# Kernel tuning notes

Measured on AMD Instinct MI355X. Metric: run time of the kernel, lower is better.

The kernel has to match this reference:

```python
import jax, jax.numpy as jnp
import numpy as np

N, E, F, B = 4096, 8192, 256, 16


def setup_inputs() -> dict:
    key = jax.random.key(0)
    k_x, k_idx, k_w, k_b = jax.random.split(key, 4)
    x = jax.random.normal(k_x, (B, E, F), dtype=jnp.float32)
    # Incidence matrix: each edge (column) connects 2 random distinct nodes.
    ends = jax.random.randint(k_idx, (2, E), 0, N)  # [2, E] node ids per edge
    cols = jnp.arange(E)
    inci = jnp.zeros((N, E), dtype=jnp.float32)
    inci = inci.at[ends[0], cols].set(1.0).at[ends[1], cols].set(1.0)
    w = jax.random.normal(k_w, (N, E), dtype=jnp.float32) * 0.05
    b = jax.random.normal(k_b, (N, E), dtype=jnp.float32) * 0.01
    return {"x": x, "inci": inci, "w": w, "b": b}


def reference(x, inci, w, b):
    # (w * inci + b) @ x : [N,E] x [B,E,F] -> [B,N,F]
    m = w * inci + b
    return jnp.einsum("ne,bef->bnf", m, x)
```

## Files before the change

### kernel.cpp

```cpp
#include <hip/hip_runtime.h>
#include <hip/hip_bf16.h>

#define Ndim 4096
#define Edim 8192
#define Fdim 256
#define Bdim 16
#define EB (Edim * 2)
#define NT (Edim / 64)

typedef __attribute__((ext_vector_type(8))) short bf16x8;
typedef __attribute__((ext_vector_type(16))) float f32x16;

__device__ __forceinline__ unsigned short f2bf(float f) {
  unsigned int u = __float_as_uint(f);
  u += 0x7fffu + ((u >> 16) & 1u);
  return (unsigned short)(u >> 16);
}

__device__ __forceinline__ void gload_lds16(const void* g, void* l) {
  __builtin_amdgcn_global_load_lds(
      (const __attribute__((address_space(1))) unsigned int*)g,
      (__attribute__((address_space(3))) unsigned int*)l, 16, 0, 0);
}

__device__ __forceinline__ void stage_half(const char* g, char* d) {
  gload_lds16(g, d);
  gload_lds16(g + (size_t)64 * EB, d + 8192);
}

#define RD32(base, r, c) \
  (*(const bf16x8*)((base) + (r) * 128 + ((((c) << 4)) ^ (((r) & 7) << 4))))

__global__ void convert_m(const float* __restrict__ w, const float* __restrict__ inc,
                          const float* __restrict__ bb, unsigned short* __restrict__ m) {
  size_t i = ((size_t)blockIdx.x * 256 + threadIdx.x) * 4;
  float4 wv = *(const float4*)(w + i);
  float4 iv = *(const float4*)(inc + i);
  float4 bv = *(const float4*)(bb + i);
  ushort4 o;
  o.x = f2bf(fmaf(wv.x, iv.x, bv.x));
  o.y = f2bf(fmaf(wv.y, iv.y, bv.y));
  o.z = f2bf(fmaf(wv.z, iv.z, bv.z));
  o.w = f2bf(fmaf(wv.w, iv.w, bv.w));
  *(ushort4*)(m + i) = o;
}

__global__ void transpose_x(const float* __restrict__ x, unsigned short* __restrict__ xT) {
  __shared__ unsigned short tile[64][66];
  int e0 = blockIdx.x * 64, f0 = blockIdx.y * 64, b = blockIdx.z;
  const float* xb = x + (size_t)b * Edim * Fdim;
  unsigned short* xTb = xT + (size_t)b * Fdim * Edim;
  int t = threadIdx.x;
  int fl = t & 63, rq = t >> 6;
#pragma unroll
  for (int i = 0; i < 16; i++) {
    int el = rq * 16 + i;
    float v = xb[(size_t)(e0 + el) * Fdim + f0 + fl];
    tile[el][fl] = f2bf(v);
  }
  __syncthreads();
  int ep = (t & 31) * 2;
  int fr0 = t >> 5;
#pragma unroll
  for (int j = 0; j < 8; j++) {
    int fr = fr0 + j * 8;
    unsigned int pk = (unsigned int)tile[ep][fr] | ((unsigned int)tile[ep + 1][fr] << 16);
    *(unsigned int*)&xTb[(size_t)(f0 + fr) * Edim + e0 + ep] = pk;
  }
}

template <int MODE>
__device__ __forceinline__ void ktile(
    const char* lA, const char* lB, const char* lAn, const char* lBn,
    char* d1, const char* g1, char* d2, const char* g2,
    char* d3, const char* g3, char* d4, const char* g4,
    int lane, int wr, int wc,
    bf16x8 (&aC)[4], bf16x8 (&bC)[2], f32x16 acc[4][2]) {
  const int l31 = lane & 31;
  const int lh = lane >> 5;
  const int rA0 = wr * 128 + l31;
  const int rB0 = wc * 64 + l31;

  if constexpr (MODE >= 1) stage_half(g1, d1);
  __builtin_amdgcn_s_barrier();
  asm volatile("s_waitcnt lgkmcnt(0)" ::: "memory");
  __builtin_amdgcn_s_setprio(1);
#pragma unroll
  for (int m = 0; m < 4; ++m)
#pragma unroll
    for (int n = 0; n < 2; ++n)
      acc[m][n] = __builtin_amdgcn_mfma_f32_32x32x16_bf16(aC[m], bC[n], acc[m][n], 0, 0, 0);
  __builtin_amdgcn_s_setprio(0);
#pragma unroll
  for (int m = 0; m < 4; ++m) aC[m] = RD32(lA, rA0 + m * 32, 2 + lh);
#pragma unroll
  for (int n = 0; n < 2; ++n) bC[n] = RD32(lB, rB0 + n * 32, 2 + lh);
  __builtin_amdgcn_s_barrier();

  if constexpr (MODE >= 1) stage_half(g2, d2);
  __builtin_amdgcn_s_barrier();
  asm volatile("s_waitcnt lgkmcnt(0)" ::: "memory");
  __builtin_amdgcn_s_setprio(1);
#pragma unroll
  for (int m = 0; m < 4; ++m)
#pragma unroll
    for (int n = 0; n < 2; ++n)
      acc[m][n] = __builtin_amdgcn_mfma_f32_32x32x16_bf16(aC[m], bC[n], acc[m][n], 0, 0, 0);
  __builtin_amdgcn_s_setprio(0);
#pragma unroll
  for (int m = 0; m < 4; ++m) aC[m] = RD32(lA, rA0 + m * 32, 4 + lh);
#pragma unroll
  for (int n = 0; n < 2; ++n) bC[n] = RD32(lB, rB0 + n * 32, 4 + lh);
  __builtin_amdgcn_s_barrier();

  __builtin_amdgcn_s_barrier();
  asm volatile("s_waitcnt lgkmcnt(0)" ::: "memory");
  __builtin_amdgcn_s_setprio(1);
#pragma unroll
  for (int m = 0; m < 4; ++m)
#pragma unroll
    for (int n = 0; n < 2; ++n)
      acc[m][n] = __builtin_amdgcn_mfma_f32_32x32x16_bf16(aC[m], bC[n], acc[m][n], 0, 0, 0);
  __builtin_amdgcn_s_setprio(0);
#pragma unroll
  for (int m = 0; m < 4; ++m) aC[m] = RD32(lA, rA0 + m * 32, 6 + lh);
#pragma unroll
  for (int n = 0; n < 2; ++n) bC[n] = RD32(lB, rB0 + n * 32, 6 + lh);
  if constexpr (MODE >= 1) asm volatile("s_waitcnt vmcnt(0)" ::: "memory");
  __builtin_amdgcn_s_barrier();

  __builtin_amdgcn_s_barrier();
  asm volatile("s_waitcnt lgkmcnt(0)" ::: "memory");
  if constexpr (MODE == 2) {
    stage_half(g3, d3);
    stage_half(g4, d4);
  }
  __builtin_amdgcn_s_setprio(1);
#pragma unroll
  for (int m = 0; m < 4; ++m)
#pragma unroll
    for (int n = 0; n < 2; ++n)
      acc[m][n] = __builtin_amdgcn_mfma_f32_32x32x16_bf16(aC[m], bC[n], acc[m][n], 0, 0, 0);
  __builtin_amdgcn_s_setprio(0);
  if constexpr (MODE >= 1) {
#pragma unroll
    for (int m = 0; m < 4; ++m) aC[m] = RD32(lAn, rA0 + m * 32, 0 + lh);
#pragma unroll
    for (int n = 0; n < 2; ++n) bC[n] = RD32(lBn, rB0 + n * 32, 0 + lh);
  }
  __builtin_amdgcn_s_barrier();
}

__global__ __launch_bounds__(512, 2) void gemm8(
    const unsigned short* __restrict__ A,
    const unsigned short* __restrict__ Bt,
    float* __restrict__ C) {
  __shared__ __align__(16) char smem[131072];

  const int bid = blockIdx.x;
  const int lid = ((bid & 7) << 5) | (bid >> 3);
  const int mt = lid >> 4;
  const int bb = lid & 15;

  const int tid = threadIdx.x;
  const int lane = tid & 63;
  const int w = tid >> 6;
  const int wr = w >> 2;
  const int wc = w & 3;
  const int l31 = lane & 31;
  const int lh = lane >> 5;

  const int r0 = tid >> 3;
  const int c0 = ((tid & 7) ^ (r0 & 7)) << 4;

  const char* Ag = (const char*)A + (size_t)(mt * 256) * EB + (size_t)r0 * EB + c0;
  const char* Bg = (const char*)Bt + (size_t)(bb * 256) * EB + (size_t)r0 * EB + c0;
  char* dst = smem + tid * 16;

  f32x16 acc[4][2];
#pragma unroll
  for (int m = 0; m < 4; ++m)
#pragma unroll
    for (int n = 0; n < 2; ++n)
#pragma unroll
      for (int r = 0; r < 16; ++r) acc[m][n][r] = 0.f;

  const size_t HEB = (size_t)128 * EB;

  stage_half(Ag, dst);
  stage_half(Ag + HEB, dst + 16384);
  stage_half(Bg, dst + 32768);
  stage_half(Bg + HEB, dst + 49152);
  stage_half(Bg + 128, dst + 98304);
  stage_half(Bg + 128 + HEB, dst + 114688);
  asm volatile("s_waitcnt vmcnt(4)" ::: "memory");
  __builtin_amdgcn_s_barrier();

  bf16x8 aC[4];
  bf16x8 bC[2];
#pragma unroll
  for (int m = 0; m < 4; ++m)
    aC[m] = RD32((const char*)smem, wr * 128 + m * 32 + l31, lh);
#pragma unroll
  for (int n = 0; n < 2; ++n)
    bC[n] = RD32((const char*)smem + 32768, wc * 64 + n * 32 + l31, lh);

  for (int i = 0; i < NT / 2 - 1; ++i) {
    const size_t t1b = (size_t)(2 * i + 1) * 128;
    const size_t t2b = (size_t)(2 * i + 2) * 128;
    const size_t t3b = (size_t)(2 * i + 3) * 128;
    ktile<2>(smem, smem + 32768, smem + 65536, smem + 98304,
             dst + 65536, Ag + t1b,
             dst + 81920, Ag + t1b + HEB,
             dst + 32768, Bg + t2b,
             dst + 49152, Bg + t2b + HEB,
             lane, wr, wc, aC, bC, acc);
    ktile<2>(smem + 65536, smem + 98304, smem, smem + 32768,
             dst, Ag + t2b,
             dst + 16384, Ag + t2b + HEB,
             dst + 98304, Bg + t3b,
             dst + 114688, Bg + t3b + HEB,
             lane, wr, wc, aC, bC, acc);
  }
  {
    const size_t tlb = (size_t)(NT - 1) * 128;
    ktile<1>(smem, smem + 32768, smem + 65536, smem + 98304,
             dst + 65536, Ag + tlb,
             dst + 81920, Ag + tlb + HEB,
             nullptr, nullptr, nullptr, nullptr,
             lane, wr, wc, aC, bC, acc);
    ktile<0>(smem + 65536, smem + 98304, nullptr, nullptr,
             nullptr, nullptr, nullptr, nullptr,
             nullptr, nullptr, nullptr, nullptr,
             lane, wr, wc, aC, bC, acc);
  }

  float* Cb = C + (size_t)bb * (Ndim * Fdim) + (size_t)(mt * 256) * Fdim;
#pragma unroll
  for (int m = 0; m < 4; ++m)
#pragma unroll
    for (int n = 0; n < 2; ++n) {
      int col = wc * 64 + n * 32 + l31;
#pragma unroll
      for (int r = 0; r < 16; ++r) {
        int row = wr * 128 + m * 32 + (r & 3) + ((r >> 2) << 3) + (lh << 2);
        Cb[(size_t)row * Fdim + col] = acc[m][n][r];
      }
    }
}

__global__ void naive_kernel(const float* __restrict__ x, const float* __restrict__ inci,
                             const float* __restrict__ w, const float* __restrict__ b,
                             float* __restrict__ out) {
  int n = blockIdx.x & (Ndim - 1);
  int bb = blockIdx.x >> 12;
  int f = threadIdx.x;
  const float* xb = x + (size_t)bb * Edim * Fdim;
  const size_t nE = (size_t)n * Edim;
  float acc = 0.f;
  for (int e = 0; e < Edim; e++) {
    float m = fmaf(w[nE + e], inci[nE + e], b[nE + e]);
    acc = fmaf(m, xb[(size_t)e * Fdim + f], acc);
  }
  out[(size_t)bb * Ndim * Fdim + (size_t)n * Fdim + f] = acc;
}

extern "C" void kernel_launch(void* const* d_in, const int* in_sizes, int n_in,
                              void* d_out, int out_size, void* d_ws, size_t ws_size,
                              hipStream_t stream) {
  const float* x = (const float*)d_in[0];
  const float* inci = (const float*)d_in[1];
  const float* w = (const float*)d_in[2];
  const float* b = (const float*)d_in[3];
  float* out = (float*)d_out;

  size_t mBytes = (size_t)Ndim * Edim * 2;
  size_t xTBytes = (size_t)Bdim * Fdim * Edim * 2;
  if (ws_size >= mBytes + xTBytes) {
    unsigned short* m_bf = (unsigned short*)d_ws;
    unsigned short* xT = m_bf + (size_t)Ndim * Edim;
    convert_m<<<(Ndim * (size_t)Edim) / 4 / 256, 256, 0, stream>>>(w, inci, b, m_bf);
    transpose_x<<<dim3(Edim / 64, Fdim / 64, Bdim), 256, 0, stream>>>(x, xT);
    gemm8<<<256, 512, 0, stream>>>(m_bf, xT, out);
  } else {
    naive_kernel<<<Bdim * Ndim, 256, 0, stream>>>(x, inci, w, b, out);
  }
}
```

Before: 346.0 us.

## Pre-pack A and B into tile-contiguous layout for linear LDS staging

The conversion kernels now write bf16 operands in a pre-tiled layout where each 64-wide k-tile of a 256-row block occupies a contiguous 32KB chunk, arranged column-chunk-major so the GEMM can stream it into LDS with linear addresses. The XOR-swizzled LDS reads are replaced with precomputed per-lane offsets, and the GEMM loop is rewritten as a single ktile per step with relaxed waits (vmcnt(4)) and fewer barriers. The aim is to cut address arithmetic and strided global loads and to improve overlap of loads with MFMA. The risk is LDS bank conflicts from the unswizzled layout, and a possible race from the removed barriers and lgkmcnt waits.

```diff
diff --git a/kernel.cpp b/kernel.cpp
--- a/kernel.cpp
+++ b/kernel.cpp
@@ -5,7 +5,6 @@
 #define Edim 8192
 #define Fdim 256
 #define Bdim 16
-#define EB (Edim * 2)
 #define NT (Edim / 64)
 
 typedef __attribute__((ext_vector_type(8))) short bf16x8;
@@ -25,135 +24,133 @@
 
 __device__ __forceinline__ void stage_half(const char* g, char* d) {
   gload_lds16(g, d);
-  gload_lds16(g + (size_t)64 * EB, d + 8192);
-}
-
-#define RD32(base, r, c) \
-  (*(const bf16x8*)((base) + (r) * 128 + ((((c) << 4)) ^ (((r) & 7) << 4))))
-
-__global__ void convert_m(const float* __restrict__ w, const float* __restrict__ inc,
-                          const float* __restrict__ bb, unsigned short* __restrict__ m) {
-  size_t i = ((size_t)blockIdx.x * 256 + threadIdx.x) * 4;
-  float4 wv = *(const float4*)(w + i);
-  float4 iv = *(const float4*)(inc + i);
-  float4 bv = *(const float4*)(bb + i);
-  ushort4 o;
-  o.x = f2bf(fmaf(wv.x, iv.x, bv.x));
-  o.y = f2bf(fmaf(wv.y, iv.y, bv.y));
-  o.z = f2bf(fmaf(wv.z, iv.z, bv.z));
-  o.w = f2bf(fmaf(wv.w, iv.w, bv.w));
-  *(ushort4*)(m + i) = o;
-}
-
-__global__ void transpose_x(const float* __restrict__ x, unsigned short* __restrict__ xT) {
-  __shared__ unsigned short tile[64][66];
-  int e0 = blockIdx.x * 64, f0 = blockIdx.y * 64, b = blockIdx.z;
+  gload_lds16(g + 8192, d + 8192);
+}
+
+#define FENCE() asm volatile("" ::: "memory")
+
+__global__ void convert_m_p(const float* __restrict__ w, const float* __restrict__ inc,
+                            const float* __restrict__ bb, unsigned short* __restrict__ Ap) {
+  const int nt = blockIdx.x;
+  const int kt = blockIdx.y;
+  const int tid = threadIdx.x;
+  const int nn = tid >> 3, c = tid & 7;
+  const int n = nt * 32 + nn;
+  const int mt = n >> 8, h = (n >> 7) & 1, r = n & 127;
+  const size_t ein = (size_t)n * Edim + kt * 64 + c * 8;
+  float4 w0 = *(const float4*)(w + ein),  w1 = *(const float4*)(w + ein + 4);
+  float4 i0 = *(const float4*)(inc + ein), i1 = *(const float4*)(inc + ein + 4);
+  float4 b0 = *(const float4*)(bb + ein),  b1 = *(const float4*)(bb + ein + 4);
+  bf16x8 o;
+  o[0] = (short)f2bf(fmaf(w0.x, i0.x, b0.x));
+  o[1] = (short)f2bf(fmaf(w0.y, i0.y, b0.y));
+  o[2] = (short)f2bf(fmaf(w0.z, i0.z, b0.z));
+  o[3] = (short)f2bf(fmaf(w0.w, i0.w, b0.w));
+  o[4] = (short)f2bf(fmaf(w1.x, i1.x, b1.x));
+  o[5] = (short)f2bf(fmaf(w1.y, i1.y, b1.y));
+  o[6] = (short)f2bf(fmaf(w1.z, i1.z, b1.z));
+  o[7] = (short)f2bf(fmaf(w1.w, i1.w, b1.w));
+  const size_t slot = ((size_t)(mt * 128 + kt) * 2 + h) * 1024 + c * 128 + r;
+  *(bf16x8*)(Ap + slot * 8) = o;
+}
+
+__global__ void transpose_x_p(const float* __restrict__ x, unsigned short* __restrict__ Bp) {
+  const int kt = blockIdx.x, f0 = blockIdx.y * 64, b = blockIdx.z;
+  const int tid = threadIdx.x;
+  const int fl = tid & 63, rq = tid >> 6;
   const float* xb = x + (size_t)b * Edim * Fdim;
-  unsigned short* xTb = xT + (size_t)b * Fdim * Edim;
-  int t = threadIdx.x;
-  int fl = t & 63, rq = t >> 6;
-#pragma unroll
-  for (int i = 0; i < 16; i++) {
-    int el = rq * 16 + i;
-    float v = xb[(size_t)(e0 + el) * Fdim + f0 + fl];
-    tile[el][fl] = f2bf(v);
-  }
-  __syncthreads();
-  int ep = (t & 31) * 2;
-  int fr0 = t >> 5;
-#pragma unroll
-  for (int j = 0; j < 8; j++) {
-    int fr = fr0 + j * 8;
-    unsigned int pk = (unsigned int)tile[ep][fr] | ((unsigned int)tile[ep + 1][fr] << 16);
-    *(unsigned int*)&xTb[(size_t)(f0 + fr) * Edim + e0 + ep] = pk;
+  const int e0 = kt * 64 + rq * 16;
+  const int f = f0 + fl;
+  unsigned short v[16];
+#pragma unroll
+  for (int i = 0; i < 16; ++i)
+    v[i] = f2bf(xb[(size_t)(e0 + i) * Fdim + f]);
+  const int h = f0 >> 7;
+  const int r = (f0 & 127) + fl;
+  const size_t base = ((size_t)(b * 128 + kt) * 2 + h) * 1024;
+#pragma unroll
+  for (int j = 0; j < 2; ++j) {
+    bf16x8 o;
+#pragma unroll
+    for (int k = 0; k < 8; ++k) o[k] = (short)v[j * 8 + k];
+    const int c = rq * 2 + j;
+    *(bf16x8*)(Bp + (base + c * 128 + r) * 8) = o;
   }
 }
 
 template <int MODE>
 __device__ __forceinline__ void ktile(
-    const char* lA, const char* lB, const char* lAn, const char* lBn,
-    char* d1, const char* g1, char* d2, const char* g2,
-    char* d3, const char* g3, char* d4, const char* g4,
-    int lane, int wr, int wc,
+    const char* cb, const char* ob,
+    char* dOther, const char* gA1,
+    char* dCur, const char* gB2,
+    const int (&aB)[4], const int (&bB)[2], const int (&cO)[4],
     bf16x8 (&aC)[4], bf16x8 (&bC)[2], f32x16 acc[4][2]) {
-  const int l31 = lane & 31;
-  const int lh = lane >> 5;
-  const int rA0 = wr * 128 + l31;
-  const int rB0 = wc * 64 + l31;
-
-  if constexpr (MODE >= 1) stage_half(g1, d1);
-  __builtin_amdgcn_s_barrier();
-  asm volatile("s_waitcnt lgkmcnt(0)" ::: "memory");
-  __builtin_amdgcn_s_setprio(1);
-#pragma unroll
-  for (int m = 0; m < 4; ++m)
-#pragma unroll
-    for (int n = 0; n < 2; ++n)
-      acc[m][n] = __builtin_amdgcn_mfma_f32_32x32x16_bf16(aC[m], bC[n], acc[m][n], 0, 0, 0);
-  __builtin_amdgcn_s_setprio(0);
-#pragma unroll
-  for (int m = 0; m < 4; ++m) aC[m] = RD32(lA, rA0 + m * 32, 2 + lh);
-#pragma unroll
-  for (int n = 0; n < 2; ++n) bC[n] = RD32(lB, rB0 + n * 32, 2 + lh);
-  __builtin_amdgcn_s_barrier();
-
-  if constexpr (MODE >= 1) stage_half(g2, d2);
-  __builtin_amdgcn_s_barrier();
-  asm volatile("s_waitcnt lgkmcnt(0)" ::: "memory");
-  __builtin_amdgcn_s_setprio(1);
-#pragma unroll
-  for (int m = 0; m < 4; ++m)
-#pragma unroll
-    for (int n = 0; n < 2; ++n)
-      acc[m][n] = __builtin_amdgcn_mfma_f32_32x32x16_bf16(aC[m], bC[n], acc[m][n], 0, 0, 0);
-  __builtin_amdgcn_s_setprio(0);
-#pragma unroll
-  for (int m = 0; m < 4; ++m) aC[m] = RD32(lA, rA0 + m * 32, 4 + lh);
-#pragma unroll
-  for (int n = 0; n < 2; ++n) bC[n] = RD32(lB, rB0 + n * 32, 4 + lh);
-  __builtin_amdgcn_s_barrier();
-
-  __builtin_amdgcn_s_barrier();
-  asm volatile("s_waitcnt lgkmcnt(0)" ::: "memory");
-  __builtin_amdgcn_s_setprio(1);
-#pragma unroll
-  for (int m = 0; m < 4; ++m)
-#pragma unroll
-    for (int n = 0; n < 2; ++n)
-      acc[m][n] = __builtin_amdgcn_mfma_f32_32x32x16_bf16(aC[m], bC[n], acc[m][n], 0, 0, 0);
-  __builtin_amdgcn_s_setprio(0);
-#pragma unroll
-  for (int m = 0; m < 4; ++m) aC[m] = RD32(lA, rA0 + m * 32, 6 + lh);
-#pragma unroll
-  for (int n = 0; n < 2; ++n) bC[n] = RD32(lB, rB0 + n * 32, 6 + lh);
-  if constexpr (MODE >= 1) asm volatile("s_waitcnt vmcnt(0)" ::: "memory");
-  __builtin_amdgcn_s_barrier();
-
-  __builtin_amdgcn_s_barrier();
-  asm volatile("s_waitcnt lgkmcnt(0)" ::: "memory");
+  if constexpr (MODE >= 1) stage_half(gA1, dOther);
+  __builtin_amdgcn_s_barrier(); FENCE();
+  __builtin_amdgcn_s_setprio(1);
+#pragma unroll
+  for (int m = 0; m < 4; ++m)
+#pragma unroll
+    for (int n = 0; n < 2; ++n)
+      acc[m][n] = __builtin_amdgcn_mfma_f32_32x32x16_bf16(aC[m], bC[n], acc[m][n], 0, 0, 0);
+  __builtin_amdgcn_s_setprio(0);
+#pragma unroll
+  for (int m = 0; m < 4; ++m) aC[m] = *(const bf16x8*)(cb + aB[m] + cO[1]);
+#pragma unroll
+  for (int n = 0; n < 2; ++n) bC[n] = *(const bf16x8*)(cb + bB[n] + cO[1]);
+
+  if constexpr (MODE >= 1) stage_half(gA1 + 16384, dOther + 16384);
+  __builtin_amdgcn_s_barrier(); FENCE();
+  __builtin_amdgcn_s_setprio(1);
+#pragma unroll
+  for (int m = 0; m < 4; ++m)
+#pragma unroll
+    for (int n = 0; n < 2; ++n)
+      acc[m][n] = __builtin_amdgcn_mfma_f32_32x32x16_bf16(aC[m], bC[n], acc[m][n], 0, 0, 0);
+  __builtin_amdgcn_s_setprio(0);
+#pragma unroll
+  for (int m = 0; m < 4; ++m) aC[m] = *(const bf16x8*)(cb + aB[m] + cO[2]);
+#pragma unroll
+  for (int n = 0; n < 2; ++n) bC[n] = *(const bf16x8*)(cb + bB[n] + cO[2]);
+
+  __builtin_amdgcn_s_barrier(); FENCE();
+  __builtin_amdgcn_s_setprio(1);
+#pragma unroll
+  for (int m = 0; m < 4; ++m)
+#pragma unroll
+    for (int n = 0; n < 2; ++n)
+      acc[m][n] = __builtin_amdgcn_mfma_f32_32x32x16_bf16(aC[m], bC[n], acc[m][n], 0, 0, 0);
+  __builtin_amdgcn_s_setprio(0);
+#pragma unroll
+  for (int m = 0; m < 4; ++m) aC[m] = *(const bf16x8*)(cb + aB[m] + cO[3]);
+#pragma unroll
+  for (int n = 0; n < 2; ++n) bC[n] = *(const bf16x8*)(cb + bB[n] + cO[3]);
+
+  __builtin_amdgcn_s_barrier(); FENCE();
   if constexpr (MODE == 2) {
-    stage_half(g3, d3);
-    stage_half(g4, d4);
-  }
-  __builtin_amdgcn_s_setprio(1);
-#pragma unroll
-  for (int m = 0; m < 4; ++m)
-#pragma unroll
-    for (int n = 0; n < 2; ++n)
-      acc[m][n] = __builtin_amdgcn_mfma_f32_32x32x16_bf16(aC[m], bC[n], acc[m][n], 0, 0, 0);
-  __builtin_amdgcn_s_setprio(0);
+    stage_half(gB2, dCur + 32768);
+    stage_half(gB2 + 16384, dCur + 49152);
+  }
+  __builtin_amdgcn_s_setprio(1);
+#pragma unroll
+  for (int m = 0; m < 4; ++m)
+#pragma unroll
+    for (int n = 0; n < 2; ++n)
+      acc[m][n] = __builtin_amdgcn_mfma_f32_32x32x16_bf16(aC[m], bC[n], acc[m][n], 0, 0, 0);
+  __builtin_amdgcn_s_setprio(0);
+  if constexpr (MODE == 2) asm volatile("s_waitcnt vmcnt(4)" ::: "memory");
+  if constexpr (MODE == 1) asm volatile("s_waitcnt vmcnt(0)" ::: "memory");
   if constexpr (MODE >= 1) {
 #pragma unroll
-    for (int m = 0; m < 4; ++m) aC[m] = RD32(lAn, rA0 + m * 32, 0 + lh);
-#pragma unroll
-    for (int n = 0; n < 2; ++n) bC[n] = RD32(lBn, rB0 + n * 32, 0 + lh);
-  }
-  __builtin_amdgcn_s_barrier();
-}
-
-__global__ __launch_bounds__(512, 2) void gemm8(
-    const unsigned short* __restrict__ A,
-    const unsigned short* __restrict__ Bt,
+    for (int m = 0; m < 4; ++m) aC[m] = *(const bf16x8*)(ob + aB[m] + cO[0]);
+#pragma unroll
+    for (int n = 0; n < 2; ++n) bC[n] = *(const bf16x8*)(ob + bB[n] + cO[0]);
+  }
+}
+
+__global__ __launch_bounds__(512, 2) void gemm32p(
+    const unsigned short* __restrict__ Ap,
+    const unsigned short* __restrict__ Bp,
     float* __restrict__ C) {
   __shared__ __align__(16) char smem[131072];
 
@@ -170,12 +167,20 @@
   const int l31 = lane & 31;
   const int lh = lane >> 5;
 
-  const int r0 = tid >> 3;
-  const int c0 = ((tid & 7) ^ (r0 & 7)) << 4;
-
-  const char* Ag = (const char*)A + (size_t)(mt * 256) * EB + (size_t)r0 * EB + c0;
-  const char* Bg = (const char*)Bt + (size_t)(bb * 256) * EB + (size_t)r0 * EB + c0;
-  char* dst = smem + tid * 16;
+  int aB[4], bB[2], cO[4];
+#pragma unroll
+  for (int m = 0; m < 4; ++m) aB[m] = wr * 16384 + (m * 32 + l31) * 16;
+#pragma unroll
+  for (int n = 0; n < 2; ++n) {
+    int rB = wc * 64 + n * 32 + l31;
+    bB[n] = 32768 + (rB >> 7) * 16384 + (rB & 127) * 16;
+  }
+#pragma unroll
+  for (int ks = 0; ks < 4; ++ks) cO[ks] = (ks * 2 + lh) * 2048;
+
+  const char* AgT = (const char*)Ap + (size_t)mt * 128 * 32768 + tid * 16;
+  const char* BgT = (const char*)Bp + (size_t)bb * 128 * 32768 + tid * 16;
+  char* dstT = smem + tid * 16;
 
   f32x16 acc[4][2];
 #pragma unroll
@@ -185,55 +190,37 @@
 #pragma unroll
       for (int r = 0; r < 16; ++r) acc[m][n][r] = 0.f;
 
-  const size_t HEB = (size_t)128 * EB;
-
-  stage_half(Ag, dst);
-  stage_half(Ag + HEB, dst + 16384);
-  stage_half(Bg, dst + 32768);
-  stage_half(Bg + HEB, dst + 49152);
-  stage_half(Bg + 128, dst + 98304);
-  stage_half(Bg + 128 + HEB, dst + 114688);
+  stage_half(AgT, dstT);
+  stage_half(AgT + 16384, dstT + 16384);
+  stage_half(BgT, dstT + 32768);
+  stage_half(BgT + 16384, dstT + 49152);
+  stage_half(BgT + 32768, dstT + 65536 + 32768);
+  stage_half(BgT + 32768 + 16384, dstT + 65536 + 49152);
   asm volatile("s_waitcnt vmcnt(4)" ::: "memory");
-  __builtin_amdgcn_s_barrier();
-
-  bf16x8 aC[4];
-  bf16x8 bC[2];
-#pragma unroll
-  for (int m = 0; m < 4; ++m)
-    aC[m] = RD32((const char*)smem, wr * 128 + m * 32 + l31, lh);
-#pragma unroll
-  for (int n = 0; n < 2; ++n)
-    bC[n] = RD32((const char*)smem + 32768, wc * 64 + n * 32 + l31, lh);
-
-  for (int i = 0; i < NT / 2 - 1; ++i) {
-    const size_t t1b = (size_t)(2 * i + 1) * 128;
-    const size_t t2b = (size_t)(2 * i + 2) * 128;
-    const size_t t3b = (size_t)(2 * i + 3) * 128;
-    ktile<2>(smem, smem + 32768, smem + 65536, smem + 98304,
-             dst + 65536, Ag + t1b,
-             dst + 81920, Ag + t1b + HEB,
-             dst + 32768, Bg + t2b,
-             dst + 49152, Bg + t2b + HEB,
-             lane, wr, wc, aC, bC, acc);
-    ktile<2>(smem + 65536, smem + 98304, smem, smem + 32768,
-             dst, Ag + t2b,
-             dst + 16384, Ag + t2b + HEB,
-             dst + 98304, Bg + t3b,
-             dst + 114688, Bg + t3b + HEB,
-             lane, wr, wc, aC, bC, acc);
-  }
-  {
-    const size_t tlb = (size_t)(NT - 1) * 128;
-    ktile<1>(smem, smem + 32768, smem + 65536, smem + 98304,
-             dst + 65536, Ag + tlb,
-             dst + 81920, Ag + tlb + HEB,
-             nullptr, nullptr, nullptr, nullptr,
-             lane, wr, wc, aC, bC, acc);
-    ktile<0>(smem + 65536, smem + 98304, nullptr, nullptr,
-             nullptr, nullptr, nullptr, nullptr,
-             nullptr, nullptr, nullptr, nullptr,
-             lane, wr, wc, aC, bC, acc);
-  }
+  __builtin_amdgcn_s_barrier(); FENCE();
+
+  bf16x8 aC[4], bC[2];
+#pragma unroll
+  for (int m = 0; m < 4; ++m) aC[m] = *(const bf16x8*)(smem + aB[m] + cO[0]);
+#pragma unroll
+  for (int n = 0; n < 2; ++n) bC[n] = *(const bf16x8*)(smem + bB[n] + cO[0]);
+
+  for (int t = 0; t < NT - 2; ++t) {
+    const int u = t & 1;
+    const char* cb = smem + u * 65536;
+    const char* ob = smem + (u ^ 1) * 65536;
+    ktile<2>(cb, ob,
+             dstT + (u ^ 1) * 65536, AgT + (size_t)(t + 1) * 32768,
+             dstT + u * 65536, BgT + (size_t)(t + 2) * 32768,
+             aB, bB, cO, aC, bC, acc);
+  }
+  ktile<1>(smem, smem + 65536,
+           dstT + 65536, AgT + (size_t)(NT - 1) * 32768,
+           dstT, nullptr,
+           aB, bB, cO, aC, bC, acc);
+  ktile<0>(smem + 65536, smem,
+           nullptr, nullptr, nullptr, nullptr,
+           aB, bB, cO, aC, bC, acc);
 
   float* Cb = C + (size_t)bb * (Ndim * Fdim) + (size_t)(mt * 256) * Fdim;
 #pragma unroll
@@ -274,14 +261,14 @@
   const float* b = (const float*)d_in[3];
   float* out = (float*)d_out;
 
-  size_t mBytes = (size_t)Ndim * Edim * 2;
-  size_t xTBytes = (size_t)Bdim * Fdim * Edim * 2;
-  if (ws_size >= mBytes + xTBytes) {
-    unsigned short* m_bf = (unsigned short*)d_ws;
-    unsigned short* xT = m_bf + (size_t)Ndim * Edim;
-    convert_m<<<(Ndim * (size_t)Edim) / 4 / 256, 256, 0, stream>>>(w, inci, b, m_bf);
-    transpose_x<<<dim3(Edim / 64, Fdim / 64, Bdim), 256, 0, stream>>>(x, xT);
-    gemm8<<<256, 512, 0, stream>>>(m_bf, xT, out);
+  size_t aBytes = (size_t)Ndim * Edim * 2;
+  size_t bBytes = (size_t)Bdim * Fdim * Edim * 2;
+  if (ws_size >= aBytes + bBytes) {
+    unsigned short* Ap = (unsigned short*)d_ws;
+    unsigned short* Bp = Ap + (size_t)Ndim * Edim;
+    convert_m_p<<<dim3(Ndim / 32, Edim / 64), 256, 0, stream>>>(w, inci, b, Ap);
+    transpose_x_p<<<dim3(Edim / 64, Fdim / 64, Bdim), 256, 0, stream>>>(x, Bp);
+    gemm32p<<<256, 512, 0, stream>>>(Ap, Bp, out);
   } else {
     naive_kernel<<<Bdim * Ndim, 256, 0, stream>>>(x, inci, w, b, out);
   }
```

Measured after the change: 366.9 us. 6.0% more time.
